# Kernel tuning notes

Measured on AMD Instinct MI355X. Metric: run time of the kernel, lower is better.

Reference implementation:

```python
import jax, jax.numpy as jnp
import numpy as np

B, N, C, H = 8, 1024, 768, 12
HD = C // H  # 64
SCALE = HD ** -0.5
T = 4
N_HALF = T // 2  # loop body with attention runs N_HALF times, V accumulates T times


def setup_inputs() -> dict:
    key = jax.random.key(0)
    ks = jax.random.split(key, 8)
    s = 0.02
    return {
        "x": jax.random.normal(ks[0], (B, N, C), jnp.float32),
        "Wqkv": jax.random.normal(ks[1], (3 * C, C), jnp.float32) * s,
        "Wfc1": jax.random.normal(ks[2], (HD, HD), jnp.float32) * s,
        "bfc1": jax.random.normal(ks[3], (HD,), jnp.float32) * s,
        "Wfc2": jax.random.normal(ks[4], (HD, HD), jnp.float32) * s,
        "bfc2": jax.random.normal(ks[5], (HD,), jnp.float32) * s,
        "Wproj": jax.random.normal(ks[6], (C, C), jnp.float32) * s,
        "bproj": jax.random.normal(ks[7], (C,), jnp.float32) * s,
    }


def reference(x, Wqkv, Wfc1, bfc1, Wfc2, bfc2, Wproj, bproj):
    b, n, c = x.shape
    # qkv projection (no bias), split into per-head q,k,v: [B,H,N,hd]
    qkv = (x @ Wqkv.T).reshape(b, n, 3, H, HD).transpose(2, 0, 3, 1, 4)
    q, k, v = qkv[0], qkv[1], qkv[2]
    # Loop body is stateless per timestep: first N_HALF steps each add the same
    # att_spk; all T steps add the same relu(v). Compute once, scale by counts.
    Q_spk = jax.nn.relu(q) @ Wfc1.T + bfc1  # [B,H,N,hd]
    K_spk = jax.nn.relu(k) @ Wfc2.T + bfc2  # [B,H,N,hd]
    att_spk = jax.nn.relu(jnp.einsum("bhqd,bhkd->bhqk", Q_spk, K_spk) * SCALE)
    att_rec = att_spk * float(N_HALF)   # accumulated over t < T/2
    V_rec = jax.nn.relu(v) * float(T)   # accumulated over all T steps
    att = jax.nn.softmax(att_rec, axis=-1)
    out = jnp.einsum("bhqk,bhkd->bhqd", att, V_rec)  # [B,H,N,hd]
    out = out.transpose(0, 2, 1, 3).reshape(b, n, c)
    return out @ Wproj.T + bproj
```

## Files before the change

kernel.cpp:

```cpp
#include <hip/hip_runtime.h>
#include <hip/hip_bf16.h>
#include <stdint.h>
#include <math.h>

#define BB   8
#define NN_  1024
#define CC   768
#define HH   12
#define HDD  64

typedef __attribute__((ext_vector_type(8))) short bf16x8;
typedef __attribute__((ext_vector_type(4))) float f32x4;
typedef __attribute__((ext_vector_type(16))) float f32x16;
typedef __attribute__((ext_vector_type(4))) float f32x4v;
typedef __attribute__((ext_vector_type(4))) unsigned short u16x4;

union FragU { unsigned int u[4]; bf16x8 b; };

__device__ __forceinline__ unsigned short f2bf(float f) {
    union { float f; unsigned int u; } v; v.f = f;
    unsigned int r = v.u + 0x7fffu + ((v.u >> 16) & 1u);
    return (unsigned short)(r >> 16);
}

#define CVTPK(d_, a_, b_) asm("v_cvt_pk_bf16_f32 %0, %1, %2" : "=v"(d_) : "v"(a_), "v"(b_))
#define SWAP32(a_, b_) asm("v_permlane32_swap_b32 %0, %1" : "+v"(a_), "+v"(b_))

__global__ void cvt4_f32_bf16(const f32x4v* __restrict__ in,
                              u16x4* __restrict__ out, int n4) {
    int i = blockIdx.x * blockDim.x + threadIdx.x;
    int stride = gridDim.x * blockDim.x;
    for (; i < n4; i += stride) {
        f32x4v v = in[i];
        u16x4 o;
        o.x = f2bf(v.x); o.y = f2bf(v.y); o.z = f2bf(v.z); o.w = f2bf(v.w);
        out[i] = o;
    }
}

__global__ __launch_bounds__(256)
void qkv_gemm(const unsigned short* __restrict__ A,
              const unsigned short* __restrict__ Bt,
              unsigned short* __restrict__ Rq,
              unsigned short* __restrict__ Rk,
              unsigned short* __restrict__ VT) {
    __shared__ short sA[128 * 32];
    __shared__ short sB[128 * 32];
    const int K = 768;
    const int lane = threadIdx.x & 63;
    const int wid  = threadIdx.x >> 6;
    const int wr = wid >> 1, wc = wid & 1;
    const int brow = blockIdx.x * 128;
    const int bcol = blockIdx.y * 128;
    const int t = threadIdx.x;

    f32x4 acc[4][4];
#pragma unroll
    for (int m = 0; m < 4; m++)
#pragma unroll
        for (int n = 0; n < 4; n++) acc[m][n] = (f32x4){0.f, 0.f, 0.f, 0.f};

    for (int k0 = 0; k0 < K; k0 += 32) {
#pragma unroll
        for (int i = 0; i < 2; i++) {
            int tt  = i * 256 + t;
            int row = tt >> 2;
            int kc  = (tt & 3) * 8;
            const unsigned short* ga = A  + (size_t)(brow + row) * K + k0 + kc;
            const unsigned short* gb = Bt + (size_t)(bcol + row) * K + k0 + kc;
            short* la = &sA[(i * 256 + wid * 64) * 8];
            short* lb = &sB[(i * 256 + wid * 64) * 8];
            __builtin_amdgcn_global_load_lds((const __attribute__((address_space(1))) void*)ga,
                                             (__attribute__((address_space(3))) void*)la, 16, 0, 0);
            __builtin_amdgcn_global_load_lds((const __attribute__((address_space(1))) void*)gb,
                                             (__attribute__((address_space(3))) void*)lb, 16, 0, 0);
        }
        __syncthreads();
        bf16x8 af[4], bfg[4];
#pragma unroll
        for (int m = 0; m < 4; m++) {
            int r = wr * 64 + m * 16 + (lane & 15);
            af[m] = *(const bf16x8*)&sA[r * 32 + (lane >> 4) * 8];
        }
#pragma unroll
        for (int n = 0; n < 4; n++) {
            int c = wc * 64 + n * 16 + (lane & 15);
            bfg[n] = *(const bf16x8*)&sB[c * 32 + (lane >> 4) * 8];
        }
#pragma unroll
        for (int m = 0; m < 4; m++)
#pragma unroll
            for (int n = 0; n < 4; n++)
                acc[m][n] = __builtin_amdgcn_mfma_f32_16x16x32_bf16(af[m], bfg[n], acc[m][n], 0, 0, 0);
        __syncthreads();
    }

    const int colbase = bcol + wc * 64;
    const int p  = colbase / 768;
    const int hh = (colbase - p * 768) >> 6;
    const int rowbase = brow + wr * 64;
    const int bb = rowbase >> 10;
    const size_t qk_base = ((size_t)(bb * HH + hh)) * NN_ * HDD;
    const size_t vt_base = ((size_t)(bb * HH + hh)) * HDD * NN_;
#pragma unroll
    for (int m = 0; m < 4; m++) {
        int nn = (rowbase + m * 16 + (lane >> 4) * 4) & (NN_ - 1);
#pragma unroll
        for (int n = 0; n < 4; n++) {
            int dd = n * 16 + (lane & 15);
#pragma unroll
            for (int r = 0; r < 4; r++) {
                float rl = fmaxf(acc[m][n][r], 0.f);
                if (p == 0)      Rq[qk_base + (size_t)(nn + r) * HDD + dd] = f2bf(rl);
                else if (p == 1) Rk[qk_base + (size_t)(nn + r) * HDD + dd] = f2bf(rl);
                else             VT[vt_base + (size_t)dd * NN_ + (nn + r)] = f2bf(4.f * rl);
            }
        }
    }
}

__global__ __launch_bounds__(256)
void spk_kernel(unsigned short* __restrict__ R,
                const unsigned short* __restrict__ W,
                const float* __restrict__ bias) {
    const int lane = threadIdx.x & 63;
    const int wid  = threadIdx.x >> 6;
    const int rowbase = blockIdx.x * 64 + wid * 16;
    const unsigned short* Arow = R + (size_t)(rowbase + (lane & 15)) * 64 + (lane >> 4) * 8;
    bf16x8 a0 = *(const bf16x8*)Arow;
    bf16x8 a1 = *(const bf16x8*)(Arow + 32);
    f32x4 acc[4];
#pragma unroll
    for (int n = 0; n < 4; n++) {
        acc[n] = (f32x4){0.f, 0.f, 0.f, 0.f};
        const unsigned short* Wrow = W + (size_t)(n * 16 + (lane & 15)) * 64 + (lane >> 4) * 8;
        bf16x8 b0 = *(const bf16x8*)Wrow;
        bf16x8 b1 = *(const bf16x8*)(Wrow + 32);
        acc[n] = __builtin_amdgcn_mfma_f32_16x16x32_bf16(a0, b0, acc[n], 0, 0, 0);
        acc[n] = __builtin_amdgcn_mfma_f32_16x16x32_bf16(a1, b1, acc[n], 0, 0, 0);
    }
#pragma unroll
    for (int n = 0; n < 4; n++) {
        int col = n * 16 + (lane & 15);
        float bv = bias[col];
#pragma unroll
        for (int r = 0; r < 4; r++) {
            int row = rowbase + (lane >> 4) * 4 + r;
            R[(size_t)row * 64 + col] = f2bf(acc[n][r] + bv);
        }
    }
}

__global__ __launch_bounds__(256, 2)
void attn_kernel(const unsigned short* __restrict__ Q,
                 const unsigned short* __restrict__ Kx,
                 const unsigned short* __restrict__ VT,
                 unsigned short* __restrict__ AO) {
    __shared__ short sK[2][64 * 64];
    __shared__ short sV[2][64 * 64];
    __shared__ float sinv[4][32];

    const int t    = threadIdx.x;
    const int lane = t & 63;
    const int wid  = t >> 6;
    const int l31  = lane & 31;
    const int hi5  = lane >> 5;

    const int bid = (int)blockIdx.x;
    const int lbid = (bid & 7) * 96 + (bid >> 3);
    const int bh = lbid >> 3;
    const int qt = lbid & 7;
    const int b = bh / HH, h = bh - b * HH;

    const unsigned short* Qs = Q  + (size_t)bh * NN_ * HDD;
    const unsigned short* Ks = Kx + (size_t)bh * NN_ * HDD;
    const unsigned short* Vt = VT + (size_t)bh * HDD * NN_;
    const int q0 = qt * 128 + wid * 32;

    bf16x8 qf[4];
#pragma unroll
    for (int ds = 0; ds < 4; ds++)
        qf[ds] = *(const bf16x8*)&Qs[(size_t)(q0 + l31) * HDD + ds * 16 + hi5 * 8];

    f32x16 O0, O1;
#pragma unroll
    for (int r = 0; r < 16; r++) { O0[r] = 0.f; O1[r] = 0.f; }
    float sumacc = 0.f;

    const int srow = t >> 3;
    const int sslot = t & 7;
    const int dstoff = ((t & 192)) * 8;

#define STAGE(buf_, kt_) do {                                                  \
    _Pragma("unroll")                                                          \
    for (int i = 0; i < 2; i++) {                                              \
        int row_ = srow + i * 32;                                              \
        int sl_  = (sslot ^ (row_ & 7)) << 3;                                  \
        const unsigned short* gk_ = Ks + (size_t)((kt_) * 64 + row_) * HDD + sl_; \
        const unsigned short* gv_ = Vt + (size_t)row_ * NN_ + (kt_) * 64 + sl_;   \
        short* dk_ = &sK[buf_][i * 2048 + dstoff];                             \
        short* dv_ = &sV[buf_][i * 2048 + dstoff];                             \
        __builtin_amdgcn_global_load_lds((const __attribute__((address_space(1))) void*)gk_, \
                                         (__attribute__((address_space(3))) void*)dk_, 16, 0, 0); \
        __builtin_amdgcn_global_load_lds((const __attribute__((address_space(1))) void*)gv_, \
                                         (__attribute__((address_space(3))) void*)dv_, 16, 0, 0); \
    }                                                                          \
} while (0)

#define MKFRAGS(P_, F0_, F1_) do {                                             \
    unsigned int c0,c1,c2,c3,c4,c5,c6,c7;                                      \
    CVTPK(c0, P_[0],  P_[1]);  CVTPK(c1, P_[2],  P_[3]);                       \
    CVTPK(c2, P_[4],  P_[5]);  CVTPK(c3, P_[6],  P_[7]);                       \
    CVTPK(c4, P_[8],  P_[9]);  CVTPK(c5, P_[10], P_[11]);                      \
    CVTPK(c6, P_[12], P_[13]); CVTPK(c7, P_[14], P_[15]);                      \
    SWAP32(c0, c2); SWAP32(c1, c3); SWAP32(c4, c6); SWAP32(c5, c7);            \
    FragU fu0_, fu1_;                                                          \
    fu0_.u[0]=c0; fu0_.u[1]=c1; fu0_.u[2]=c2; fu0_.u[3]=c3;                    \
    fu1_.u[0]=c4; fu1_.u[1]=c5; fu1_.u[2]=c6; fu1_.u[3]=c7;                    \
    F0_ = fu0_.b; F1_ = fu1_.b;                                                \
} while (0)

    STAGE(0, 0);
    __syncthreads();

    int buf = 0;
    for (int kt = 0; kt < 16; ++kt) {
        if (kt < 15) STAGE(buf ^ 1, kt + 1);

        const char* kbase = (const char*)&sK[buf][0];
        const char* vbase = (const char*)&sV[buf][0];

        bf16x8 vbf[4][2];
#pragma unroll
        for (int ks = 0; ks < 4; ks++)
#pragma unroll
            for (int dt = 0; dt < 2; dt++) {
                int d = dt * 32 + l31;
                vbf[ks][dt] = *(const bf16x8*)(vbase + d * 128 +
                               ((ks * 32 + hi5 * 16) ^ ((d & 7) << 4)));
            }
        bf16x8 ka[2][4];
#pragma unroll
        for (int kt2 = 0; kt2 < 2; kt2++)
#pragma unroll
            for (int ds = 0; ds < 4; ds++) {
                int kk = kt2 * 32 + l31;
                ka[kt2][ds] = *(const bf16x8*)(kbase + kk * 128 +
                               ((ds * 32 + hi5 * 16) ^ ((kk & 7) << 4)));
            }

        f32x16 S0, S1;
#pragma unroll
        for (int r = 0; r < 16; r++) { S0[r] = 0.f; S1[r] = 0.f; }
#pragma unroll
        for (int ds = 0; ds < 4; ds++) {
            S0 = __builtin_amdgcn_mfma_f32_32x32x16_bf16(ka[0][ds], qf[ds], S0, 0, 0, 0);
            S1 = __builtin_amdgcn_mfma_f32_32x32x16_bf16(ka[1][ds], qf[ds], S1, 0, 0, 0);
        }

        float p0[16], p1[16];
#pragma unroll
        for (int r = 0; r < 16; r++) {
            p0[r] = exp2f(0.36067376f * fmaxf(S0[r], 0.f));
            p1[r] = exp2f(0.36067376f * fmaxf(S1[r], 0.f));
        }
        float s0 = 0.f, s1 = 0.f;
#pragma unroll
        for (int r = 0; r < 16; r++) { s0 += p0[r]; s1 += p1[r]; }
        sumacc += s0 + s1;

        bf16x8 paf0, paf1, paf2, paf3;
        MKFRAGS(p0, paf0, paf1);
        MKFRAGS(p1, paf2, paf3);

        O0 = __builtin_amdgcn_mfma_f32_32x32x16_bf16(paf0, vbf[0][0], O0, 0, 0, 0);
        O1 = __builtin_amdgcn_mfma_f32_32x32x16_bf16(paf0, vbf[0][1], O1, 0, 0, 0);
        O0 = __builtin_amdgcn_mfma_f32_32x32x16_bf16(paf1, vbf[1][0], O0, 0, 0, 0);
        O1 = __builtin_amdgcn_mfma_f32_32x32x16_bf16(paf1, vbf[1][1], O1, 0, 0, 0);
        O0 = __builtin_amdgcn_mfma_f32_32x32x16_bf16(paf2, vbf[2][0], O0, 0, 0, 0);
        O1 = __builtin_amdgcn_mfma_f32_32x32x16_bf16(paf2, vbf[2][1], O1, 0, 0, 0);
        O0 = __builtin_amdgcn_mfma_f32_32x32x16_bf16(paf3, vbf[3][0], O0, 0, 0, 0);
        O1 = __builtin_amdgcn_mfma_f32_32x32x16_bf16(paf3, vbf[3][1], O1, 0, 0, 0);

        __syncthreads();
        buf ^= 1;
    }
#undef STAGE
#undef MKFRAGS

    float stot = sumacc + __shfl_xor(sumacc, 32, 64);
    float inv = 1.f / stot;
    if (l31 == lane) sinv[wid][l31] = inv;
    __syncthreads();

#pragma unroll
    for (int r = 0; r < 16; r++) {
        int qloc = (r & 3) + 8 * (r >> 2) + 4 * hi5;
        float iv = sinv[wid][qloc];
        size_t row = (size_t)(b * NN_ + q0 + qloc) * CC + h * HDD;
        AO[row + l31]      = f2bf(O0[r] * iv);
        AO[row + 32 + l31] = f2bf(O1[r] * iv);
    }
}

__global__ __launch_bounds__(256)
void proj_gemm(const unsigned short* __restrict__ A,
               const unsigned short* __restrict__ Bt,
               const float* __restrict__ bias,
               float* __restrict__ Out) {
    __shared__ short sA[128 * 32];
    __shared__ short sB[128 * 32];
    const int K = 768;
    const int lane = threadIdx.x & 63;
    const int wid  = threadIdx.x >> 6;
    const int wr = wid >> 1, wc = wid & 1;
    const int brow = blockIdx.x * 128;
    const int bcol = blockIdx.y * 128;
    const int t = threadIdx.x;

    f32x4 acc[4][4];
#pragma unroll
    for (int m = 0; m < 4; m++)
#pragma unroll
        for (int n = 0; n < 4; n++) acc[m][n] = (f32x4){0.f, 0.f, 0.f, 0.f};

    for (int k0 = 0; k0 < K; k0 += 32) {
#pragma unroll
        for (int i = 0; i < 2; i++) {
            int tt  = i * 256 + t;
            int row = tt >> 2;
            int kc  = (tt & 3) * 8;
            const unsigned short* ga = A  + (size_t)(brow + row) * K + k0 + kc;
            const unsigned short* gb = Bt + (size_t)(bcol + row) * K + k0 + kc;
            short* la = &sA[(i * 256 + wid * 64) * 8];
            short* lb = &sB[(i * 256 + wid * 64) * 8];
            __builtin_amdgcn_global_load_lds((const __attribute__((address_space(1))) void*)ga,
                                             (__attribute__((address_space(3))) void*)la, 16, 0, 0);
            __builtin_amdgcn_global_load_lds((const __attribute__((address_space(1))) void*)gb,
                                             (__attribute__((address_space(3))) void*)lb, 16, 0, 0);
        }
        __syncthreads();
        bf16x8 af[4], bfg[4];
#pragma unroll
        for (int m = 0; m < 4; m++) {
            int r = wr * 64 + m * 16 + (lane & 15);
            af[m] = *(const bf16x8*)&sA[r * 32 + (lane >> 4) * 8];
        }
#pragma unroll
        for (int n = 0; n < 4; n++) {
            int c = wc * 64 + n * 16 + (lane & 15);
            bfg[n] = *(const bf16x8*)&sB[c * 32 + (lane >> 4) * 8];
        }
#pragma unroll
        for (int m = 0; m < 4; m++)
#pragma unroll
            for (int n = 0; n < 4; n++)
                acc[m][n] = __builtin_amdgcn_mfma_f32_16x16x32_bf16(af[m], bfg[n], acc[m][n], 0, 0, 0);
        __syncthreads();
    }
#pragma unroll
    for (int m = 0; m < 4; m++)
#pragma unroll
        for (int n = 0; n < 4; n++) {
            int col = bcol + wc * 64 + n * 16 + (lane & 15);
            float bv = bias[col];
#pragma unroll
            for (int r = 0; r < 4; r++) {
                int row = brow + wr * 64 + m * 16 + (lane >> 4) * 4 + r;
                Out[(size_t)row * 768 + col] = acc[m][n][r] + bv;
            }
        }
}

extern "C" void kernel_launch(void* const* d_in, const int* in_sizes, int n_in,
                              void* d_out, int out_size, void* d_ws, size_t ws_size,
                              hipStream_t stream) {
    const float* x     = (const float*)d_in[0];
    const float* Wqkv  = (const float*)d_in[1];
    const float* Wfc1  = (const float*)d_in[2];
    const float* bfc1  = (const float*)d_in[3];
    const float* Wfc2  = (const float*)d_in[4];
    const float* bfc2  = (const float*)d_in[5];
    const float* Wproj = (const float*)d_in[6];
    const float* bproj = (const float*)d_in[7];
    float* out = (float*)d_out;

    char* ws = (char*)d_ws;
    const size_t SZ_XN = (size_t)8192 * 768 * 2;
    unsigned short* x_bf    = (unsigned short*)ws; ws += SZ_XN;
    unsigned short* wqkv_bf = (unsigned short*)ws; ws += (size_t)2304 * 768 * 2;
    unsigned short* wproj_bf= (unsigned short*)ws; ws += (size_t)768 * 768 * 2;
    unsigned short* wfc1_bf = (unsigned short*)ws; ws += 64 * 64 * 2;
    unsigned short* wfc2_bf = (unsigned short*)ws; ws += 64 * 64 * 2;
    unsigned short* Rq      = (unsigned short*)ws; ws += SZ_XN;
    unsigned short* Rk      = (unsigned short*)ws; ws += SZ_XN;
    unsigned short* VT      = (unsigned short*)ws; ws += SZ_XN;

    cvt4_f32_bf16<<<2048, 256, 0, stream>>>((const f32x4v*)x,     (u16x4*)x_bf,     8192 * 768 / 4);
    cvt4_f32_bf16<<<1024, 256, 0, stream>>>((const f32x4v*)Wqkv,  (u16x4*)wqkv_bf,  2304 * 768 / 4);
    cvt4_f32_bf16<<<576,  256, 0, stream>>>((const f32x4v*)Wproj, (u16x4*)wproj_bf, 768 * 768 / 4);
    cvt4_f32_bf16<<<4,    256, 0, stream>>>((const f32x4v*)Wfc1,  (u16x4*)wfc1_bf,  64 * 64 / 4);
    cvt4_f32_bf16<<<4,    256, 0, stream>>>((const f32x4v*)Wfc2,  (u16x4*)wfc2_bf,  64 * 64 / 4);

    qkv_gemm<<<dim3(64, 18), 256, 0, stream>>>(x_bf, wqkv_bf, Rq, Rk, VT);
    spk_kernel<<<1536, 256, 0, stream>>>(Rq, wfc1_bf, bfc1);
    spk_kernel<<<1536, 256, 0, stream>>>(Rk, wfc2_bf, bfc2);
    attn_kernel<<<768, 256, 0, stream>>>(Rq, Rk, VT, x_bf);
    proj_gemm<<<dim3(64, 6), 256, 0, stream>>>(x_bf, wproj_bf, bproj, out);
}
```

Before: 164.7 us.

## Fuse spike projections into QKV GEMM epilogue and merge conversion kernels

Five separate f32-to-bf16 conversion launches are merged into one kernel, and the two spk_kernel passes are folded into the QKV GEMM epilogue. The relu'd Q/K tiles are repacked into MFMA fragments and multiplied by the 64x64 fc weights in registers before a single write. The QKV GEMM also moves to 32x32x16 MFMAs with an XOR-swizzled LDS layout. The aim is to cut launch overhead and the extra global read/write round trip of Rq/Rk, at the cost of more register pressure in the GEMM epilogue.

```diff
diff --git a/kernel.cpp b/kernel.cpp
--- a/kernel.cpp
+++ b/kernel.cpp
@@ -26,186 +26,9 @@
 #define CVTPK(d_, a_, b_) asm("v_cvt_pk_bf16_f32 %0, %1, %2" : "=v"(d_) : "v"(a_), "v"(b_))
 #define SWAP32(a_, b_) asm("v_permlane32_swap_b32 %0, %1" : "+v"(a_), "+v"(b_))
 
-__global__ void cvt4_f32_bf16(const f32x4v* __restrict__ in,
-                              u16x4* __restrict__ out, int n4) {
-    int i = blockIdx.x * blockDim.x + threadIdx.x;
-    int stride = gridDim.x * blockDim.x;
-    for (; i < n4; i += stride) {
-        f32x4v v = in[i];
-        u16x4 o;
-        o.x = f2bf(v.x); o.y = f2bf(v.y); o.z = f2bf(v.z); o.w = f2bf(v.w);
-        out[i] = o;
-    }
-}
-
-__global__ __launch_bounds__(256)
-void qkv_gemm(const unsigned short* __restrict__ A,
-              const unsigned short* __restrict__ Bt,
-              unsigned short* __restrict__ Rq,
-              unsigned short* __restrict__ Rk,
-              unsigned short* __restrict__ VT) {
-    __shared__ short sA[128 * 32];
-    __shared__ short sB[128 * 32];
-    const int K = 768;
-    const int lane = threadIdx.x & 63;
-    const int wid  = threadIdx.x >> 6;
-    const int wr = wid >> 1, wc = wid & 1;
-    const int brow = blockIdx.x * 128;
-    const int bcol = blockIdx.y * 128;
-    const int t = threadIdx.x;
-
-    f32x4 acc[4][4];
-#pragma unroll
-    for (int m = 0; m < 4; m++)
-#pragma unroll
-        for (int n = 0; n < 4; n++) acc[m][n] = (f32x4){0.f, 0.f, 0.f, 0.f};
-
-    for (int k0 = 0; k0 < K; k0 += 32) {
-#pragma unroll
-        for (int i = 0; i < 2; i++) {
-            int tt  = i * 256 + t;
-            int row = tt >> 2;
-            int kc  = (tt & 3) * 8;
-            const unsigned short* ga = A  + (size_t)(brow + row) * K + k0 + kc;
-            const unsigned short* gb = Bt + (size_t)(bcol + row) * K + k0 + kc;
-            short* la = &sA[(i * 256 + wid * 64) * 8];
-            short* lb = &sB[(i * 256 + wid * 64) * 8];
-            __builtin_amdgcn_global_load_lds((const __attribute__((address_space(1))) void*)ga,
-                                             (__attribute__((address_space(3))) void*)la, 16, 0, 0);
-            __builtin_amdgcn_global_load_lds((const __attribute__((address_space(1))) void*)gb,
-                                             (__attribute__((address_space(3))) void*)lb, 16, 0, 0);
-        }
-        __syncthreads();
-        bf16x8 af[4], bfg[4];
-#pragma unroll
-        for (int m = 0; m < 4; m++) {
-            int r = wr * 64 + m * 16 + (lane & 15);
-            af[m] = *(const bf16x8*)&sA[r * 32 + (lane >> 4) * 8];
-        }
-#pragma unroll
-        for (int n = 0; n < 4; n++) {
-            int c = wc * 64 + n * 16 + (lane & 15);
-            bfg[n] = *(const bf16x8*)&sB[c * 32 + (lane >> 4) * 8];
-        }
-#pragma unroll
-        for (int m = 0; m < 4; m++)
-#pragma unroll
-            for (int n = 0; n < 4; n++)
-                acc[m][n] = __builtin_amdgcn_mfma_f32_16x16x32_bf16(af[m], bfg[n], acc[m][n], 0, 0, 0);
-        __syncthreads();
-    }
-
-    const int colbase = bcol + wc * 64;
-    const int p  = colbase / 768;
-    const int hh = (colbase - p * 768) >> 6;
-    const int rowbase = brow + wr * 64;
-    const int bb = rowbase >> 10;
-    const size_t qk_base = ((size_t)(bb * HH + hh)) * NN_ * HDD;
-    const size_t vt_base = ((size_t)(bb * HH + hh)) * HDD * NN_;
-#pragma unroll
-    for (int m = 0; m < 4; m++) {
-        int nn = (rowbase + m * 16 + (lane >> 4) * 4) & (NN_ - 1);
-#pragma unroll
-        for (int n = 0; n < 4; n++) {
-            int dd = n * 16 + (lane & 15);
-#pragma unroll
-            for (int r = 0; r < 4; r++) {
-                float rl = fmaxf(acc[m][n][r], 0.f);
-                if (p == 0)      Rq[qk_base + (size_t)(nn + r) * HDD + dd] = f2bf(rl);
-                else if (p == 1) Rk[qk_base + (size_t)(nn + r) * HDD + dd] = f2bf(rl);
-                else             VT[vt_base + (size_t)dd * NN_ + (nn + r)] = f2bf(4.f * rl);
-            }
-        }
-    }
-}
-
-__global__ __launch_bounds__(256)
-void spk_kernel(unsigned short* __restrict__ R,
-                const unsigned short* __restrict__ W,
-                const float* __restrict__ bias) {
-    const int lane = threadIdx.x & 63;
-    const int wid  = threadIdx.x >> 6;
-    const int rowbase = blockIdx.x * 64 + wid * 16;
-    const unsigned short* Arow = R + (size_t)(rowbase + (lane & 15)) * 64 + (lane >> 4) * 8;
-    bf16x8 a0 = *(const bf16x8*)Arow;
-    bf16x8 a1 = *(const bf16x8*)(Arow + 32);
-    f32x4 acc[4];
-#pragma unroll
-    for (int n = 0; n < 4; n++) {
-        acc[n] = (f32x4){0.f, 0.f, 0.f, 0.f};
-        const unsigned short* Wrow = W + (size_t)(n * 16 + (lane & 15)) * 64 + (lane >> 4) * 8;
-        bf16x8 b0 = *(const bf16x8*)Wrow;
-        bf16x8 b1 = *(const bf16x8*)(Wrow + 32);
-        acc[n] = __builtin_amdgcn_mfma_f32_16x16x32_bf16(a0, b0, acc[n], 0, 0, 0);
-        acc[n] = __builtin_amdgcn_mfma_f32_16x16x32_bf16(a1, b1, acc[n], 0, 0, 0);
-    }
-#pragma unroll
-    for (int n = 0; n < 4; n++) {
-        int col = n * 16 + (lane & 15);
-        float bv = bias[col];
-#pragma unroll
-        for (int r = 0; r < 4; r++) {
-            int row = rowbase + (lane >> 4) * 4 + r;
-            R[(size_t)row * 64 + col] = f2bf(acc[n][r] + bv);
-        }
-    }
-}
-
-__global__ __launch_bounds__(256, 2)
-void attn_kernel(const unsigned short* __restrict__ Q,
-                 const unsigned short* __restrict__ Kx,
-                 const unsigned short* __restrict__ VT,
-                 unsigned short* __restrict__ AO) {
-    __shared__ short sK[2][64 * 64];
-    __shared__ short sV[2][64 * 64];
-    __shared__ float sinv[4][32];
-
-    const int t    = threadIdx.x;
-    const int lane = t & 63;
-    const int wid  = t >> 6;
-    const int l31  = lane & 31;
-    const int hi5  = lane >> 5;
-
-    const int bid = (int)blockIdx.x;
-    const int lbid = (bid & 7) * 96 + (bid >> 3);
-    const int bh = lbid >> 3;
-    const int qt = lbid & 7;
-    const int b = bh / HH, h = bh - b * HH;
-
-    const unsigned short* Qs = Q  + (size_t)bh * NN_ * HDD;
-    const unsigned short* Ks = Kx + (size_t)bh * NN_ * HDD;
-    const unsigned short* Vt = VT + (size_t)bh * HDD * NN_;
-    const int q0 = qt * 128 + wid * 32;
-
-    bf16x8 qf[4];
-#pragma unroll
-    for (int ds = 0; ds < 4; ds++)
-        qf[ds] = *(const bf16x8*)&Qs[(size_t)(q0 + l31) * HDD + ds * 16 + hi5 * 8];
-
-    f32x16 O0, O1;
-#pragma unroll
-    for (int r = 0; r < 16; r++) { O0[r] = 0.f; O1[r] = 0.f; }
-    float sumacc = 0.f;
-
-    const int srow = t >> 3;
-    const int sslot = t & 7;
-    const int dstoff = ((t & 192)) * 8;
-
-#define STAGE(buf_, kt_) do {                                                  \
-    _Pragma("unroll")                                                          \
-    for (int i = 0; i < 2; i++) {                                              \
-        int row_ = srow + i * 32;                                              \
-        int sl_  = (sslot ^ (row_ & 7)) << 3;                                  \
-        const unsigned short* gk_ = Ks + (size_t)((kt_) * 64 + row_) * HDD + sl_; \
-        const unsigned short* gv_ = Vt + (size_t)row_ * NN_ + (kt_) * 64 + sl_;   \
-        short* dk_ = &sK[buf_][i * 2048 + dstoff];                             \
-        short* dv_ = &sV[buf_][i * 2048 + dstoff];                             \
-        __builtin_amdgcn_global_load_lds((const __attribute__((address_space(1))) void*)gk_, \
-                                         (__attribute__((address_space(3))) void*)dk_, 16, 0, 0); \
-        __builtin_amdgcn_global_load_lds((const __attribute__((address_space(1))) void*)gv_, \
-                                         (__attribute__((address_space(3))) void*)dv_, 16, 0, 0); \
-    }                                                                          \
-} while (0)
+#define GLDS(g_, l_) __builtin_amdgcn_global_load_lds( \
+    (const __attribute__((address_space(1))) void*)(g_), \
+    (__attribute__((address_space(3))) void*)(l_), 16, 0, 0)
 
 #define MKFRAGS(P_, F0_, F1_) do {                                             \
     unsigned int c0,c1,c2,c3,c4,c5,c6,c7;                                      \
@@ -220,6 +43,229 @@
     F0_ = fu0_.b; F1_ = fu1_.b;                                                \
 } while (0)
 
+#define CVT_N0 1572864
+#define CVT_N1 2015232
+#define CVT_N2 2162688
+#define CVT_N3 2163712
+#define CVT_N4 2164736
+__global__ void cvt_all(const float* __restrict__ x, const float* __restrict__ wqkv,
+                        const float* __restrict__ wproj, const float* __restrict__ wf1,
+                        const float* __restrict__ wf2,
+                        unsigned short* __restrict__ xb, unsigned short* __restrict__ wqkvb,
+                        unsigned short* __restrict__ wprojb, unsigned short* __restrict__ wf1b,
+                        unsigned short* __restrict__ wf2b) {
+    int i = blockIdx.x * blockDim.x + threadIdx.x;
+    int stride = gridDim.x * blockDim.x;
+    for (; i < CVT_N4; i += stride) {
+        const f32x4v* src; u16x4* dst; int off;
+        if (i < CVT_N0)      { src = (const f32x4v*)x;     dst = (u16x4*)xb;     off = i; }
+        else if (i < CVT_N1) { src = (const f32x4v*)wqkv;  dst = (u16x4*)wqkvb;  off = i - CVT_N0; }
+        else if (i < CVT_N2) { src = (const f32x4v*)wproj; dst = (u16x4*)wprojb; off = i - CVT_N1; }
+        else if (i < CVT_N3) { src = (const f32x4v*)wf1;   dst = (u16x4*)wf1b;   off = i - CVT_N2; }
+        else                 { src = (const f32x4v*)wf2;   dst = (u16x4*)wf2b;   off = i - CVT_N3; }
+        f32x4v v = src[off];
+        u16x4 o;
+        o.x = f2bf(v.x); o.y = f2bf(v.y); o.z = f2bf(v.z); o.w = f2bf(v.w);
+        dst[off] = o;
+    }
+}
+
+__global__ __launch_bounds__(256)
+void qkv_spk_gemm(const unsigned short* __restrict__ X,
+                  const unsigned short* __restrict__ Wqkv,
+                  const unsigned short* __restrict__ Wf1,
+                  const unsigned short* __restrict__ Wf2,
+                  const float* __restrict__ bf1,
+                  const float* __restrict__ bf2,
+                  unsigned short* __restrict__ Rq,
+                  unsigned short* __restrict__ Rk,
+                  unsigned short* __restrict__ VT) {
+    __shared__ short sX[128 * 32];
+    __shared__ short sW[128 * 32];
+    const int K = 768;
+    const int t    = threadIdx.x;
+    const int wid  = t >> 6;
+    const int lane = t & 63;
+    const int l31  = lane & 31;
+    const int hi5  = lane >> 5;
+    const int th = (wid & 1) * 64;
+    const int fh = (wid >> 1) * 64;
+    const int brow = blockIdx.x * 128;
+    const int bcol = blockIdx.y * 128;
+
+    const int srow = t >> 2;
+    const int scol = ((t & 3) ^ (srow & 3)) * 8;
+
+#define QSTG(k0_) do {                                                         \
+    _Pragma("unroll")                                                          \
+    for (int i = 0; i < 2; i++) {                                              \
+        int row_ = srow + i * 64;                                              \
+        GLDS(X    + (size_t)(brow + row_) * K + (k0_) + scol,                  \
+             &sX[(i * 256 + wid * 64) * 8]);                                   \
+        GLDS(Wqkv + (size_t)(bcol + row_) * K + (k0_) + scol,                  \
+             &sW[(i * 256 + wid * 64) * 8]);                                   \
+    }                                                                          \
+} while (0)
+
+    f32x16 acc[2][2];
+#pragma unroll
+    for (int fb = 0; fb < 2; fb++)
+#pragma unroll
+        for (int tb = 0; tb < 2; tb++)
+#pragma unroll
+            for (int r = 0; r < 16; r++) acc[fb][tb][r] = 0.f;
+
+    for (int k0 = 0; k0 < K; k0 += 32) {
+        QSTG(k0);
+        __syncthreads();
+        const char* cw = (const char*)sW;
+        const char* cx = (const char*)sX;
+        bf16x8 wf[2][2], xf[2][2];
+#pragma unroll
+        for (int fb = 0; fb < 2; fb++) {
+            int row = fh + fb * 32 + l31;
+            const char* rb = cw + row * 64;
+#pragma unroll
+            for (int kk = 0; kk < 2; kk++)
+                wf[fb][kk] = *(const bf16x8*)(rb + (((kk * 2 + hi5) ^ (row & 3)) << 4));
+        }
+#pragma unroll
+        for (int tb = 0; tb < 2; tb++) {
+            int row = th + tb * 32 + l31;
+            const char* rb = cx + row * 64;
+#pragma unroll
+            for (int kk = 0; kk < 2; kk++)
+                xf[tb][kk] = *(const bf16x8*)(rb + (((kk * 2 + hi5) ^ (row & 3)) << 4));
+        }
+#pragma unroll
+        for (int kk = 0; kk < 2; kk++)
+#pragma unroll
+            for (int fb = 0; fb < 2; fb++)
+#pragma unroll
+                for (int tb = 0; tb < 2; tb++)
+                    acc[fb][tb] = __builtin_amdgcn_mfma_f32_32x32x16_bf16(
+                        wf[fb][kk], xf[tb][kk], acc[fb][tb], 0, 0, 0);
+        __syncthreads();
+    }
+#undef QSTG
+
+    const int fbase = bcol + fh;
+    const int p  = fbase / 768;
+    const int hh = (fbase - p * 768) >> 6;
+    const int tok0 = brow + th;
+    const int b  = tok0 >> 10;
+    const int n0 = tok0 & 1023;
+    const int crow0 = 4 * hi5;
+
+    if (p == 2) {
+        const size_t vtb = ((size_t)(b * HH + hh)) * HDD * NN_;
+#pragma unroll
+        for (int fb = 0; fb < 2; fb++)
+#pragma unroll
+            for (int tb = 0; tb < 2; tb++)
+#pragma unroll
+                for (int r = 0; r < 16; r++) {
+                    int d = fb * 32 + (r & 3) + 8 * (r >> 2) + crow0;
+                    int n = n0 + tb * 32 + l31;
+                    VT[vtb + (size_t)d * NN_ + n] = f2bf(4.f * fmaxf(acc[fb][tb][r], 0.f));
+                }
+    } else {
+        const unsigned short* Wf = p ? Wf2 : Wf1;
+        const float* bfp = p ? bf2 : bf1;
+        unsigned short* R = p ? Rk : Rq;
+        bf16x8 wfr[2][4];
+#pragma unroll
+        for (int dh = 0; dh < 2; dh++)
+#pragma unroll
+            for (int ks = 0; ks < 4; ks++)
+                wfr[dh][ks] = *(const bf16x8*)&Wf[(size_t)(dh * 32 + l31) * HDD + ks * 16 + hi5 * 8];
+        float bv0 = bfp[l31], bv1 = bfp[32 + l31];
+        const size_t qkb = ((size_t)(b * HH + hh)) * NN_ * HDD;
+#pragma unroll
+        for (int tb = 0; tb < 2; tb++) {
+            float pv0[16], pv1[16];
+#pragma unroll
+            for (int r = 0; r < 16; r++) {
+                pv0[r] = fmaxf(acc[0][tb][r], 0.f);
+                pv1[r] = fmaxf(acc[1][tb][r], 0.f);
+            }
+            bf16x8 pa0, pa1, pa2, pa3;
+            MKFRAGS(pv0, pa0, pa1);
+            MKFRAGS(pv1, pa2, pa3);
+            f32x16 D0, D1;
+#pragma unroll
+            for (int r = 0; r < 16; r++) { D0[r] = 0.f; D1[r] = 0.f; }
+            D0 = __builtin_amdgcn_mfma_f32_32x32x16_bf16(pa0, wfr[0][0], D0, 0, 0, 0);
+            D0 = __builtin_amdgcn_mfma_f32_32x32x16_bf16(pa1, wfr[0][1], D0, 0, 0, 0);
+            D0 = __builtin_amdgcn_mfma_f32_32x32x16_bf16(pa2, wfr[0][2], D0, 0, 0, 0);
+            D0 = __builtin_amdgcn_mfma_f32_32x32x16_bf16(pa3, wfr[0][3], D0, 0, 0, 0);
+            D1 = __builtin_amdgcn_mfma_f32_32x32x16_bf16(pa0, wfr[1][0], D1, 0, 0, 0);
+            D1 = __builtin_amdgcn_mfma_f32_32x32x16_bf16(pa1, wfr[1][1], D1, 0, 0, 0);
+            D1 = __builtin_amdgcn_mfma_f32_32x32x16_bf16(pa2, wfr[1][2], D1, 0, 0, 0);
+            D1 = __builtin_amdgcn_mfma_f32_32x32x16_bf16(pa3, wfr[1][3], D1, 0, 0, 0);
+#pragma unroll
+            for (int r = 0; r < 16; r++) {
+                int n = n0 + tb * 32 + (r & 3) + 8 * (r >> 2) + crow0;
+                size_t rowb = qkb + (size_t)n * HDD;
+                R[rowb + l31]      = f2bf(D0[r] + bv0);
+                R[rowb + 32 + l31] = f2bf(D1[r] + bv1);
+            }
+        }
+    }
+}
+
+__global__ __launch_bounds__(256, 2)
+void attn_kernel(const unsigned short* __restrict__ Q,
+                 const unsigned short* __restrict__ Kx,
+                 const unsigned short* __restrict__ VT,
+                 unsigned short* __restrict__ AO) {
+    __shared__ short sK[2][64 * 64];
+    __shared__ short sV[2][64 * 64];
+    __shared__ float sinv[4][32];
+
+    const int t    = threadIdx.x;
+    const int lane = t & 63;
+    const int wid  = t >> 6;
+    const int l31  = lane & 31;
+    const int hi5  = lane >> 5;
+
+    const int bid = (int)blockIdx.x;
+    const int lbid = (bid & 7) * 96 + (bid >> 3);
+    const int bh = lbid >> 3;
+    const int qt = lbid & 7;
+    const int b = bh / HH, h = bh - b * HH;
+
+    const unsigned short* Qs = Q  + (size_t)bh * NN_ * HDD;
+    const unsigned short* Ks = Kx + (size_t)bh * NN_ * HDD;
+    const unsigned short* Vt = VT + (size_t)bh * HDD * NN_;
+    const int q0 = qt * 128 + wid * 32;
+
+    bf16x8 qf[4];
+#pragma unroll
+    for (int ds = 0; ds < 4; ds++)
+        qf[ds] = *(const bf16x8*)&Qs[(size_t)(q0 + l31) * HDD + ds * 16 + hi5 * 8];
+
+    f32x16 O0, O1;
+#pragma unroll
+    for (int r = 0; r < 16; r++) { O0[r] = 0.f; O1[r] = 0.f; }
+    float sumacc = 0.f;
+
+    const int srow = t >> 3;
+    const int sslot = t & 7;
+    const int dstoff = ((t & 192)) * 8;
+
+#define STAGE(buf_, kt_) do {                                                  \
+    _Pragma("unroll")                                                          \
+    for (int i = 0; i < 2; i++) {                                              \
+        int row_ = srow + i * 32;                                              \
+        int sl_  = (sslot ^ (row_ & 7)) << 3;                                  \
+        const unsigned short* gk_ = Ks + (size_t)((kt_) * 64 + row_) * HDD + sl_; \
+        const unsigned short* gv_ = Vt + (size_t)row_ * NN_ + (kt_) * 64 + sl_;   \
+        GLDS(gk_, &sK[buf_][i * 2048 + dstoff]);                               \
+        GLDS(gv_, &sV[buf_][i * 2048 + dstoff]);                               \
+    }                                                                          \
+} while (0)
+
     STAGE(0, 0);
     __syncthreads();
 
@@ -286,7 +332,6 @@
         buf ^= 1;
     }
 #undef STAGE
-#undef MKFRAGS
 
     float stot = sumacc + __shfl_xor(sumacc, 32, 64);
     float inv = 1.f / stot;
@@ -332,12 +377,8 @@
             int kc  = (tt & 3) * 8;
             const unsigned short* ga = A  + (size_t)(brow + row) * K + k0 + kc;
             const unsigned short* gb = Bt + (size_t)(bcol + row) * K + k0 + kc;
-            short* la = &sA[(i * 256 + wid * 64) * 8];
-            short* lb = &sB[(i * 256 + wid * 64) * 8];
-            __builtin_amdgcn_global_load_lds((const __attribute__((address_space(1))) void*)ga,
-                                             (__attribute__((address_space(3))) void*)la, 16, 0, 0);
-            __builtin_amdgcn_global_load_lds((const __attribute__((address_space(1))) void*)gb,
-                                             (__attribute__((address_space(3))) void*)lb, 16, 0, 0);
+            GLDS(ga, &sA[(i * 256 + wid * 64) * 8]);
+            GLDS(gb, &sB[(i * 256 + wid * 64) * 8]);
         }
         __syncthreads();
         bf16x8 af[4], bfg[4];
@@ -396,15 +437,10 @@
     unsigned short* Rk      = (unsigned short*)ws; ws += SZ_XN;
     unsigned short* VT      = (unsigned short*)ws; ws += SZ_XN;
 
-    cvt4_f32_bf16<<<2048, 256, 0, stream>>>((const f32x4v*)x,     (u16x4*)x_bf,     8192 * 768 / 4);
-    cvt4_f32_bf16<<<1024, 256, 0, stream>>>((const f32x4v*)Wqkv,  (u16x4*)wqkv_bf,  2304 * 768 / 4);
-    cvt4_f32_bf16<<<576,  256, 0, stream>>>((const f32x4v*)Wproj, (u16x4*)wproj_bf, 768 * 768 / 4);
-    cvt4_f32_bf16<<<4,    256, 0, stream>>>((const f32x4v*)Wfc1,  (u16x4*)wfc1_bf,  64 * 64 / 4);
-    cvt4_f32_bf16<<<4,    256, 0, stream>>>((const f32x4v*)Wfc2,  (u16x4*)wfc2_bf,  64 * 64 / 4);
-
-    qkv_gemm<<<dim3(64, 18), 256, 0, stream>>>(x_bf, wqkv_bf, Rq, Rk, VT);
-    spk_kernel<<<1536, 256, 0, stream>>>(Rq, wfc1_bf, bfc1);
-    spk_kernel<<<1536, 256, 0, stream>>>(Rk, wfc2_bf, bfc2);
+    cvt_all<<<2048, 256, 0, stream>>>(x, Wqkv, Wproj, Wfc1, Wfc2,
+                                      x_bf, wqkv_bf, wproj_bf, wfc1_bf, wfc2_bf);
+    qkv_spk_gemm<<<dim3(64, 18), 256, 0, stream>>>(x_bf, wqkv_bf, wfc1_bf, wfc2_bf,
+                                                   bfc1, bfc2, Rq, Rk, VT);
     attn_kernel<<<768, 256, 0, stream>>>(Rq, Rk, VT, x_bf);
     proj_gemm<<<dim3(64, 6), 256, 0, stream>>>(x_bf, wproj_bf, bproj, out);
 }
```

New measurement: 144.9 us. -12.0%, faster.
